# Kernel tuning notes

Measured on AMD Instinct MI355X. Metric: run time of the kernel, lower is better.

The kernel has to match this reference:

```python
import jax, jax.numpy as jnp
import numpy as np

BATCH_SEQ = 16384
D_MODEL = 2048
NUM_EXPERTS = 64
TOP_K = 2
NOISE_STD = 0.1
AUX_LOSS_WEIGHT = 0.001


def setup_inputs() -> dict:
    key = jax.random.key(0)
    k1, k2, k3 = jax.random.split(key, 3)
    hidden_states = jax.random.normal(k1, (BATCH_SEQ, D_MODEL), dtype=jnp.float32)
    router_weight = jax.random.normal(k2, (NUM_EXPERTS, D_MODEL), dtype=jnp.float32) * 0.02
    noise = jax.random.normal(k3, (BATCH_SEQ, NUM_EXPERTS), dtype=jnp.float32)
    return {"hidden_states": hidden_states, "router_weight": router_weight, "noise": noise}


def reference(hidden_states, router_weight, noise):
    # router logits: [batch_seq, num_experts] (temperature == 1.0 -> no scaling)
    router_logits = jnp.einsum("td,ed->te", hidden_states, router_weight)
    router_logits = router_logits + noise * NOISE_STD

    # top-k selection and softmax over the selected logits
    expert_weights, expert_indices = jax.lax.top_k(router_logits, TOP_K)
    expert_weights = jax.nn.softmax(expert_weights, axis=-1)

    # aux load-balancing loss
    routing_probs = jax.nn.softmax(router_logits, axis=-1)  # [t, e]
    expert_mask = jax.nn.one_hot(expert_indices, NUM_EXPERTS, dtype=jnp.float32).sum(axis=1)  # [t, e]
    expert_usage = expert_mask.sum(axis=0) / (BATCH_SEQ * TOP_K)  # [e]
    mean_routing_prob = routing_probs.mean(axis=0)  # [e]
    aux_loss = (expert_usage * mean_routing_prob).sum() * NUM_EXPERTS * AUX_LOSS_WEIGHT

    return expert_indices, expert_weights, router_logits, aux_loss
```

## Files before the change

kernel.cpp:

```cpp
#include <hip/hip_runtime.h>
#include <math.h>

#define BATCH 16384
#define DM    2048
#define NE    64
#define BT    32
#define DK    32
#define NBLK  (BATCH / BT)

#define OFF_W   32768
#define OFF_LG  65536
#define OFF_AUX 1114112

#define WS_USAGE (NBLK * NE)

__global__ __launch_bounds__(256) void router_kernel(
    const float* __restrict__ H, const float* __restrict__ W,
    const float* __restrict__ NZ, float* __restrict__ out,
    float* __restrict__ ws)
{
    __shared__ float hs [DK * 36];
    __shared__ float wsm[DK * 68];
    __shared__ float ps [16 * 68];
    __shared__ int   cnt[NE];

    const int tid = threadIdx.x;
    const int blk = blockIdx.x;
    const int er  = tid & 15;
    const int tr  = tid >> 4;
    const int e4  = er << 2;
    const int t2  = tr << 1;

    float a00=0,a01=0,a02=0,a03=0, a10=0,a11=0,a12=0,a13=0;

    const float* hb = H + (size_t)blk * BT * DM;
    const int ht = tid >> 3;
    const int hd = (tid & 7) << 2;

    for (int d0 = 0; d0 < DM; d0 += DK) {
        float4 hv = *(const float4*)(hb + (size_t)ht * DM + d0 + hd);
        float4 w0 = *(const float4*)(W  + (size_t)ht        * DM + d0 + hd);
        float4 w1 = *(const float4*)(W  + (size_t)(ht + 32) * DM + d0 + hd);
        hs[(hd+0)*36 + ht] = hv.x;
        hs[(hd+1)*36 + ht] = hv.y;
        hs[(hd+2)*36 + ht] = hv.z;
        hs[(hd+3)*36 + ht] = hv.w;
        wsm[(hd+0)*68 + ht] = w0.x;
        wsm[(hd+1)*68 + ht] = w0.y;
        wsm[(hd+2)*68 + ht] = w0.z;
        wsm[(hd+3)*68 + ht] = w0.w;
        wsm[(hd+0)*68 + ht+32] = w1.x;
        wsm[(hd+1)*68 + ht+32] = w1.y;
        wsm[(hd+2)*68 + ht+32] = w1.z;
        wsm[(hd+3)*68 + ht+32] = w1.w;
        __syncthreads();
        #pragma unroll
        for (int dd = 0; dd < DK; ++dd) {
            const float2 av = *(const float2*)(hs  + dd*36 + t2);
            const float4 bv = *(const float4*)(wsm + dd*68 + e4);
            a00 += av.x*bv.x; a01 += av.x*bv.y; a02 += av.x*bv.z; a03 += av.x*bv.w;
            a10 += av.y*bv.x; a11 += av.y*bv.y; a12 += av.y*bv.z; a13 += av.y*bv.w;
        }
        __syncthreads();
    }

    float l[2][4];
    {
        size_t tg0 = (size_t)blk * BT + t2;
        float4 n0 = *(const float4*)(NZ + tg0 * NE + e4);
        float4 n1 = *(const float4*)(NZ + (tg0 + 1) * NE + e4);
        l[0][0] = a00 + n0.x*0.1f; l[0][1] = a01 + n0.y*0.1f;
        l[0][2] = a02 + n0.z*0.1f; l[0][3] = a03 + n0.w*0.1f;
        l[1][0] = a10 + n1.x*0.1f; l[1][1] = a11 + n1.y*0.1f;
        l[1][2] = a12 + n1.z*0.1f; l[1][3] = a13 + n1.w*0.1f;
        *(float4*)(out + OFF_LG + tg0 * NE + e4)       = make_float4(l[0][0],l[0][1],l[0][2],l[0][3]);
        *(float4*)(out + OFF_LG + (tg0 + 1) * NE + e4) = make_float4(l[1][0],l[1][1],l[1][2],l[1][3]);
    }
    if (tid < NE) cnt[tid] = 0;
    __syncthreads();

    float pe0 = 0.f, pe1 = 0.f, pe2 = 0.f, pe3 = 0.f;
    #pragma unroll
    for (int i = 0; i < 2; ++i) {
        float m1 = l[i][0]; int i1 = e4;
        float m2 = -INFINITY; int i2 = NE;
        #pragma unroll
        for (int j = 1; j < 4; ++j) {
            float v = l[i][j]; int e = e4 + j;
            if (v > m1) { m2 = m1; i2 = i1; m1 = v; i1 = e; }
            else if (v > m2) { m2 = v; i2 = e; }
        }
        #pragma unroll
        for (int mask = 1; mask < 16; mask <<= 1) {
            float om1 = __shfl_xor(m1, mask);
            int   oi1 = __shfl_xor(i1, mask);
            float om2 = __shfl_xor(m2, mask);
            int   oi2 = __shfl_xor(i2, mask);
            bool oFirst = (om1 > m1) || (om1 == m1 && oi1 < i1);
            if (oFirst) {
                bool selfSecond = (m1 > om2) || (m1 == om2 && i1 < oi2);
                m2 = selfSecond ? m1 : om2;
                i2 = selfSecond ? i1 : oi2;
                m1 = om1; i1 = oi1;
            } else {
                bool otherSecond = (om1 > m2) || (om1 == m2 && oi1 < i2);
                if (otherSecond) { m2 = om1; i2 = oi1; }
            }
        }
        float p0 = expf(l[i][0] - m1);
        float p1 = expf(l[i][1] - m1);
        float p2 = expf(l[i][2] - m1);
        float p3 = expf(l[i][3] - m1);
        float s = p0 + p1 + p2 + p3;
        #pragma unroll
        for (int mask = 1; mask < 16; mask <<= 1) s += __shfl_xor(s, mask);
        float inv = 1.0f / s;
        pe0 += p0*inv; pe1 += p1*inv; pe2 += p2*inv; pe3 += p3*inv;
        if (er == 0) {
            size_t tg = (size_t)blk * BT + t2 + i;
            out[tg*2 + 0] = (float)i1;
            out[tg*2 + 1] = (float)i2;
            float x  = expf(m2 - m1);
            float w1v = 1.0f / (1.0f + x);
            out[OFF_W + tg*2 + 0] = w1v;
            out[OFF_W + tg*2 + 1] = x * w1v;
            atomicAdd(&cnt[i1], 1);
            atomicAdd(&cnt[i2], 1);
        }
    }
    ps[tr*68 + e4 + 0] = pe0;
    ps[tr*68 + e4 + 1] = pe1;
    ps[tr*68 + e4 + 2] = pe2;
    ps[tr*68 + e4 + 3] = pe3;
    __syncthreads();

    if (tid < NE) {
        float s = 0.f;
        #pragma unroll
        for (int r = 0; r < 16; ++r) s += ps[r*68 + tid];
        ws[(size_t)blk * NE + tid] = s;
        ws[WS_USAGE + (size_t)blk * NE + tid] = (float)cnt[tid];
    }
}

__global__ __launch_bounds__(256) void finalize_kernel(
    const float* __restrict__ ws, float* __restrict__ out)
{
    __shared__ float psum[256];
    __shared__ float usum[256];
    const int tid  = threadIdx.x;
    const int e    = tid & 63;
    const int part = tid >> 6;
    float p = 0.f, u = 0.f;
    for (int b = part * 128; b < part * 128 + 128; ++b) {
        p += ws[(size_t)b * NE + e];
        u += ws[WS_USAGE + (size_t)b * NE + e];
    }
    psum[part*64 + e] = p;
    usum[part*64 + e] = u;
    __syncthreads();
    if (tid < 64) {
        float pv = psum[tid] + psum[64+tid] + psum[128+tid] + psum[192+tid];
        float uv = usum[tid] + usum[64+tid] + usum[128+tid] + usum[192+tid];
        float v = (uv / (float)(BATCH * 2)) * (pv / (float)BATCH);
        #pragma unroll
        for (int mask = 1; mask < 64; mask <<= 1) v += __shfl_xor(v, mask);
        if (tid == 0) out[OFF_AUX] = v * ((float)NE * 0.001f);
    }
}

extern "C" void kernel_launch(void* const* d_in, const int* in_sizes, int n_in,
                              void* d_out, int out_size, void* d_ws, size_t ws_size,
                              hipStream_t stream)
{
    const float* H  = (const float*)d_in[0];
    const float* W  = (const float*)d_in[1];
    const float* NZ = (const float*)d_in[2];
    float* out = (float*)d_out;
    float* ws  = (float*)d_ws;

    router_kernel<<<dim3(NBLK), dim3(256), 0, stream>>>(H, W, NZ, out, ws);
    finalize_kernel<<<dim3(1), dim3(256), 0, stream>>>(ws, out);
}
```

Before: 300.6 us.

## Use 4x8 register tiles with split-K across wavefronts and larger K chunks

The GEMM loop now stages 128-wide K chunks in shared memory instead of 32. Each thread computes a 4x8 output tile rather than 2x4, and the four wavefronts each take a quarter of every chunk. The split-K partial sums are then combined in shared memory through a serialized four-step reduction before the top-k and softmax epilogue. This is meant to raise FMA work per shared-memory load and cut the number of barriers, at the cost of more LDS, more registers and an extra reduction phase.

```diff
diff --git a/kernel.cpp b/kernel.cpp
--- a/kernel.cpp
+++ b/kernel.cpp
@@ -5,7 +5,7 @@
 #define DM    2048
 #define NE    64
 #define BT    32
-#define DK    32
+#define DKC   128
 #define NBLK  (BATCH / BT)
 
 #define OFF_W   32768
@@ -13,66 +13,114 @@
 #define OFF_AUX 1114112
 
 #define WS_USAGE (NBLK * NE)
+
+#define HS_S 36
+#define WS_S 68
 
 __global__ __launch_bounds__(256) void router_kernel(
     const float* __restrict__ H, const float* __restrict__ W,
     const float* __restrict__ NZ, float* __restrict__ out,
     float* __restrict__ ws)
 {
-    __shared__ float hs [DK * 36];
-    __shared__ float wsm[DK * 68];
-    __shared__ float ps [16 * 68];
-    __shared__ int   cnt[NE];
-
-    const int tid = threadIdx.x;
-    const int blk = blockIdx.x;
-    const int er  = tid & 15;
-    const int tr  = tid >> 4;
-    const int e4  = er << 2;
-    const int t2  = tr << 1;
-
-    float a00=0,a01=0,a02=0,a03=0, a10=0,a11=0,a12=0,a13=0;
+    __shared__ float hs  [DKC * HS_S];
+    __shared__ float wsm [DKC * WS_S];
+    __shared__ float lred[BT * 68];
+    __shared__ float ps  [16 * 68];
+    __shared__ int   cnt [NE];
+
+    const int tid  = threadIdx.x;
+    const int blk  = blockIdx.x;
+    const int kg   = tid >> 6;
+    const int lane = tid & 63;
+    const int eg   = lane & 7;
+    const int tg   = lane >> 3;
+    const int e8   = eg << 3;
+    const int t4g  = tg << 2;
+
+    float acc[4][8];
+    #pragma unroll
+    for (int i = 0; i < 4; ++i)
+        #pragma unroll
+        for (int j = 0; j < 8; ++j) acc[i][j] = 0.f;
 
     const float* hb = H + (size_t)blk * BT * DM;
-    const int ht = tid >> 3;
-    const int hd = (tid & 7) << 2;
-
-    for (int d0 = 0; d0 < DM; d0 += DK) {
-        float4 hv = *(const float4*)(hb + (size_t)ht * DM + d0 + hd);
-        float4 w0 = *(const float4*)(W  + (size_t)ht        * DM + d0 + hd);
-        float4 w1 = *(const float4*)(W  + (size_t)(ht + 32) * DM + d0 + hd);
-        hs[(hd+0)*36 + ht] = hv.x;
-        hs[(hd+1)*36 + ht] = hv.y;
-        hs[(hd+2)*36 + ht] = hv.z;
-        hs[(hd+3)*36 + ht] = hv.w;
-        wsm[(hd+0)*68 + ht] = w0.x;
-        wsm[(hd+1)*68 + ht] = w0.y;
-        wsm[(hd+2)*68 + ht] = w0.z;
-        wsm[(hd+3)*68 + ht] = w0.w;
-        wsm[(hd+0)*68 + ht+32] = w1.x;
-        wsm[(hd+1)*68 + ht+32] = w1.y;
-        wsm[(hd+2)*68 + ht+32] = w1.z;
-        wsm[(hd+3)*68 + ht+32] = w1.w;
+
+    for (int c = 0; c < DM / DKC; ++c) {
+        const int D0 = c * DKC;
+        #pragma unroll
+        for (int p = 0; p < 4; ++p) {
+            int f  = p * 256 + tid;
+            int t  = (f >> 3) & 31;
+            int d4 = ((f >> 8) << 5) + ((f & 7) << 2);
+            float4 v = *(const float4*)(hb + (size_t)t * DM + D0 + d4);
+            hs[(d4+0)*HS_S + t] = v.x;
+            hs[(d4+1)*HS_S + t] = v.y;
+            hs[(d4+2)*HS_S + t] = v.z;
+            hs[(d4+3)*HS_S + t] = v.w;
+        }
+        #pragma unroll
+        for (int p = 0; p < 8; ++p) {
+            int f  = p * 256 + tid;
+            int e  = (f >> 3) & 63;
+            int d4 = ((f >> 9) << 5) + ((f & 7) << 2);
+            float4 v = *(const float4*)(W + (size_t)e * DM + D0 + d4);
+            wsm[(d4+0)*WS_S + e] = v.x;
+            wsm[(d4+1)*WS_S + e] = v.y;
+            wsm[(d4+2)*WS_S + e] = v.z;
+            wsm[(d4+3)*WS_S + e] = v.w;
+        }
         __syncthreads();
-        #pragma unroll
-        for (int dd = 0; dd < DK; ++dd) {
-            const float2 av = *(const float2*)(hs  + dd*36 + t2);
-            const float4 bv = *(const float4*)(wsm + dd*68 + e4);
-            a00 += av.x*bv.x; a01 += av.x*bv.y; a02 += av.x*bv.z; a03 += av.x*bv.w;
-            a10 += av.y*bv.x; a11 += av.y*bv.y; a12 += av.y*bv.z; a13 += av.y*bv.w;
+        #pragma unroll 8
+        for (int dd = 0; dd < 32; ++dd) {
+            const int d = (kg << 5) + dd;
+            const float4 a  = *(const float4*)(hs  + d*HS_S + t4g);
+            const float4 b0 = *(const float4*)(wsm + d*WS_S + e8);
+            const float4 b1 = *(const float4*)(wsm + d*WS_S + e8 + 4);
+            const float av[4] = {a.x, a.y, a.z, a.w};
+            const float bv[8] = {b0.x,b0.y,b0.z,b0.w,b1.x,b1.y,b1.z,b1.w};
+            #pragma unroll
+            for (int i = 0; i < 4; ++i)
+                #pragma unroll
+                for (int j = 0; j < 8; ++j)
+                    acc[i][j] += av[i] * bv[j];
         }
         __syncthreads();
     }
+
+    #pragma unroll
+    for (int g = 0; g < 4; ++g) {
+        if (kg == g) {
+            #pragma unroll
+            for (int i = 0; i < 4; ++i) {
+                float* row = lred + (t4g + i) * 68 + e8;
+                if (g == 0) {
+                    #pragma unroll
+                    for (int j = 0; j < 8; ++j) row[j] = acc[i][j];
+                } else {
+                    #pragma unroll
+                    for (int j = 0; j < 8; ++j) row[j] += acc[i][j];
+                }
+            }
+        }
+        __syncthreads();
+    }
+
+    const int er = tid & 15;
+    const int tr = tid >> 4;
+    const int e4 = er << 2;
+    const int t2 = tr << 1;
 
     float l[2][4];
     {
         size_t tg0 = (size_t)blk * BT + t2;
         float4 n0 = *(const float4*)(NZ + tg0 * NE + e4);
         float4 n1 = *(const float4*)(NZ + (tg0 + 1) * NE + e4);
-        l[0][0] = a00 + n0.x*0.1f; l[0][1] = a01 + n0.y*0.1f;
-        l[0][2] = a02 + n0.z*0.1f; l[0][3] = a03 + n0.w*0.1f;
-        l[1][0] = a10 + n1.x*0.1f; l[1][1] = a11 + n1.y*0.1f;
-        l[1][2] = a12 + n1.z*0.1f; l[1][3] = a13 + n1.w*0.1f;
+        float4 a0 = *(const float4*)(lred + (t2+0)*68 + e4);
+        float4 a1 = *(const float4*)(lred + (t2+1)*68 + e4);
+        l[0][0] = a0.x + n0.x*0.1f; l[0][1] = a0.y + n0.y*0.1f;
+        l[0][2] = a0.z + n0.z*0.1f; l[0][3] = a0.w + n0.w*0.1f;
+        l[1][0] = a1.x + n1.x*0.1f; l[1][1] = a1.y + n1.y*0.1f;
+        l[1][2] = a1.z + n1.z*0.1f; l[1][3] = a1.w + n1.w*0.1f;
         *(float4*)(out + OFF_LG + tg0 * NE + e4)       = make_float4(l[0][0],l[0][1],l[0][2],l[0][3]);
         *(float4*)(out + OFF_LG + (tg0 + 1) * NE + e4) = make_float4(l[1][0],l[1][1],l[1][2],l[1][3]);
     }
@@ -117,13 +165,13 @@
         float inv = 1.0f / s;
         pe0 += p0*inv; pe1 += p1*inv; pe2 += p2*inv; pe3 += p3*inv;
         if (er == 0) {
-            size_t tg = (size_t)blk * BT + t2 + i;
-            out[tg*2 + 0] = (float)i1;
-            out[tg*2 + 1] = (float)i2;
-            float x  = expf(m2 - m1);
+            size_t tgi = (size_t)blk * BT + t2 + i;
+            out[tgi*2 + 0] = (float)i1;
+            out[tgi*2 + 1] = (float)i2;
+            float x   = expf(m2 - m1);
             float w1v = 1.0f / (1.0f + x);
-            out[OFF_W + tg*2 + 0] = w1v;
-            out[OFF_W + tg*2 + 1] = x * w1v;
+            out[OFF_W + tgi*2 + 0] = w1v;
+            out[OFF_W + tgi*2 + 1] = x * w1v;
             atomicAdd(&cnt[i1], 1);
             atomicAdd(&cnt[i2], 1);
         }
```

Measured after the change: 263.9 us. 12.2% less time.
